# Kernel tuning notes

Hardware: AMD Instinct MI355X
Metric: run time of the kernel (lower is better)

The kernel has to match this reference:

```python
import jax, jax.numpy as jnp
import numpy as np
import math

STRIDES = [4, 8, 16, 32, 64]
SCALES  = [32, 64, 128, 256, 512]
RATIOS  = [2.0, 1.0, 0.5]
GRIDS   = [(200, 304), (100, 152), (50, 76), (25, 38), (13, 19)]  # 800x1216 canvas
LSZ     = [gh * gw * 3 for gh, gw in GRIDS]                        # anchors per level
PRE_NMS_K = [min(1000, n) for n in LSZ]                            # select_by_score (1000, lsz)
IMG_H, IMG_W = 800, 1216
BBOX_CLAMP = math.log(1000.0 / 16.0)
IOU_TH = 0.7
MAX_OUT = 1000
MIN_SIZE = 1e-2
LEVEL_OFFSET = 1e4  # batched-NMS level separation offset


def _make_priors():
    # post.get_priors with loc='corner': anchor centers at stride*i (no +0.5)
    out = []
    for st, (gh, gw), sc in zip(STRIDES, GRIDS, SCALES):
        anc = []
        for r in RATIOS:  # make_anchors_rounded: 1 scale x 3 ratios, rounded
            h = sc * np.sqrt(r)
            w = sc / np.sqrt(r)
            anc.append(np.round(np.array([-w / 2, -h / 2, w / 2, h / 2])))
        anc = np.stack(anc)  # [3,4]
        ys = (np.arange(gh) * st).astype(np.float32)
        xs = (np.arange(gw) * st).astype(np.float32)
        yy, xx = np.meshgrid(ys, xs, indexing='ij')
        shifts = np.stack([xx, yy, xx, yy], axis=-1).reshape(-1, 1, 4)  # [gh*gw,1,4]
        out.append((shifts + anc[None].astype(np.float32)).reshape(-1, 4))
    return np.concatenate(out).astype(np.float32)  # [A,4]


def setup_inputs() -> dict:
    key = jax.random.key(0)
    k1, k2 = jax.random.split(key)
    B, A = 16, sum(LSZ)
    reg = jax.random.normal(k1, (B, A, 4), dtype=jnp.float32) * 0.5  # box deltas
    obj = jax.random.normal(k2, (B, A, 1), dtype=jnp.float32)        # objectness logits
    priors = jnp.asarray(_make_priors())
    return {"reg": reg, "obj": obj, "priors": priors}


def _nms(boxes, init_keep):
    # sequential NMS over score-sorted boxes; boxes already level-offset. [N,4]
    N = boxes.shape[0]
    areas = jnp.clip(boxes[:, 2] - boxes[:, 0], 0) * jnp.clip(boxes[:, 3] - boxes[:, 1], 0)
    rng = jnp.arange(N)

    def body(i, keep):
        b = boxes[i]
        xx1 = jnp.maximum(b[0], boxes[:, 0])
        yy1 = jnp.maximum(b[1], boxes[:, 1])
        xx2 = jnp.minimum(b[2], boxes[:, 2])
        yy2 = jnp.minimum(b[3], boxes[:, 3])
        inter = jnp.clip(xx2 - xx1, 0) * jnp.clip(yy2 - yy1, 0)
        iou = inter / (areas[i] + areas - inter + 1e-9)
        sup = (iou > IOU_TH) & (rng > i) & keep[i]
        return keep & ~sup

    return jax.lax.fori_loop(0, N, body, init_keep)


def reference(reg, obj, priors):
    B = reg.shape[0]
    scores = jax.nn.sigmoid(obj[..., 0])  # [B,A]

    # per-level top-k selection (select_by_score with (1000, lsz))
    off = 0
    idxs, scs, levs = [], [], []
    for l, (n, k) in enumerate(zip(LSZ, PRE_NMS_K)):
        sv, si = jax.lax.top_k(scores[:, off:off + n], k)
        idxs.append(si + off)
        scs.append(sv)
        levs.append(np.full(k, l, np.int32))
        off += n
    idx = jnp.concatenate(idxs, axis=1)       # [B,N] global anchor indices
    sc = jnp.concatenate(scs, axis=1)         # [B,N]
    levels = jnp.asarray(np.concatenate(levs))  # [N]

    reg_s = jnp.take_along_axis(reg, idx[..., None], axis=1)  # [B,N,4]
    pri_s = priors[idx]                                        # [B,N,4]

    # decode_boxes, settings=(1, 1, log(1000/16))
    pw = pri_s[..., 2] - pri_s[..., 0]
    ph = pri_s[..., 3] - pri_s[..., 1]
    pcx = pri_s[..., 0] + 0.5 * pw
    pcy = pri_s[..., 1] + 0.5 * ph
    dx, dy = reg_s[..., 0], reg_s[..., 1]
    dw = jnp.minimum(reg_s[..., 2], BBOX_CLAMP)
    dh = jnp.minimum(reg_s[..., 3], BBOX_CLAMP)
    cx = dx * pw + pcx
    cy = dy * ph + pcy
    w = pw * jnp.exp(dw)
    h = ph * jnp.exp(dh)
    boxes = jnp.stack([cx - 0.5 * w, cy - 0.5 * h, cx + 0.5 * w, cy + 0.5 * h], axis=-1)

    # clamp_to_canvas
    boxes = jnp.stack([
        jnp.clip(boxes[..., 0], 0, IMG_W), jnp.clip(boxes[..., 1], 0, IMG_H),
        jnp.clip(boxes[..., 2], 0, IMG_W), jnp.clip(boxes[..., 3], 0, IMG_H)], axis=-1)

    # remove_small
    small_ok = ((boxes[..., 2] - boxes[..., 0]) > MIN_SIZE) & ((boxes[..., 3] - boxes[..., 1]) > MIN_SIZE)

    # global score-descending order for NMS
    order = jnp.argsort(-sc, axis=1)
    boxes = jnp.take_along_axis(boxes, order[..., None], axis=1)
    sc = jnp.take_along_axis(sc, order, axis=1)
    small_ok = jnp.take_along_axis(small_ok, order, axis=1)
    lev = jnp.take_along_axis(jnp.broadcast_to(levels, sc.shape), order, axis=1)

    # per-level batched NMS via coordinate offset; NMS decisions are non-differentiable
    boxes_off = jax.lax.stop_gradient(boxes) + lev[..., None].astype(boxes.dtype) * LEVEL_OFFSET
    keep = jax.vmap(_nms)(boxes_off, small_ok)  # [B,N] bool

    # take first MAX_OUT kept (already score-sorted), pad with zeros
    rank = jnp.cumsum(keep, axis=1) - 1
    pos = jnp.where(keep & (rank < MAX_OUT), rank, MAX_OUT)  # dump slot MAX_OUT
    out_b = jax.vmap(lambda p, b: jnp.zeros((MAX_OUT + 1, 4), b.dtype).at[p].set(b))(pos, boxes)[:, :MAX_OUT]
    out_s = jax.vmap(lambda p, s: jnp.zeros((MAX_OUT + 1,), s.dtype).at[p].set(s))(pos, sc)[:, :MAX_OUT]
    return jnp.concatenate([out_b, out_s[..., None]], axis=-1)  # [B,1000,5]
```

## Files before the change

kernel.cpp:

```cpp
#include <hip/hip_runtime.h>

typedef unsigned int u32;
typedef unsigned short u16;
typedef unsigned long long u64;

#define NB 16
#define NA 242991
#define NSEL 4741

__device__ __constant__ int c_LN[5]   = {182400, 45600, 11400, 2850, 741};
__device__ __constant__ int c_LOFF[5] = {0, 182400, 228000, 239400, 242250};
__device__ __constant__ int c_LK[5]   = {1000, 1000, 1000, 1000, 741};
__device__ __constant__ int c_SOFF[5] = {0, 1000, 2000, 3000, 4000};
__device__ __constant__ int c_CST[5]  = {0, 64, 80, 84, 85};
__device__ __constant__ int c_CCN[5]  = {64, 16, 4, 1, 1};


__device__ __forceinline__ float xla_tanhf(float x) {
#pragma clang fp contract(off)
  float t = fminf(fmaxf(x, -9.0f), 9.0f);
  float x2 = t * t;
  float p = -2.76076847742355e-16f;
  p = p * x2 + 2.00018790482477e-13f;
  p = p * x2 + -8.60467152213735e-11f;
  p = p * x2 + 5.12229709037114e-08f;
  p = p * x2 + 1.48572235717979e-05f;
  p = p * x2 + 6.37261928875436e-04f;
  p = p * x2 + 4.89352455891786e-03f;
  p = t * p;
  float q = 1.19825839466702e-06f;
  q = q * x2 + 1.18534705686654e-04f;
  q = q * x2 + 2.26843463243900e-03f;
  q = q * x2 + 4.89352518554385e-03f;
  float r = p / q;
  return (fabsf(x) < 0.0004f) ? x : r;
}

__device__ __forceinline__ float ref_sigmoid(float x) {
#pragma clang fp contract(off)
  float t = 0.5f * x;
  float th = xla_tanhf(t);
  return 0.5f + 0.5f * th;
}

__device__ __forceinline__ float xla_expf(float x) {
#pragma clang fp contract(off)
  float fx = x * 1.44269504088896341f + 0.5f;
  fx = floorf(fx);
  float tmp = fx * 0.693359375f;
  float z = fx * -2.12194440e-4f;
  float r = x - tmp;
  r = r - z;
  float r2 = r * r;
  float y = 1.9875691500e-4f;
  y = y * r + 1.3981999507e-3f;
  y = y * r + 8.3334519073e-3f;
  y = y * r + 4.1665795894e-2f;
  y = y * r + 1.6666665459e-1f;
  y = y * r + 5.0000001201e-1f;
  y = y * r2 + r;
  y = y + 1.0f;
  int k = (int)fx;
  float two_k = __uint_as_float((u32)((k + 127) << 23));
  return y * two_k;
}

__device__ __forceinline__ void chunk_map(int c, int& l, int& base, int& n) {
  if (c < 64)      { l = 0; base = c * 2850;                 n = 2850; }
  else if (c < 80) { l = 1; base = 182400 + (c - 64) * 2850; n = 2850; }
  else if (c < 84) { l = 2; base = 228000 + (c - 80) * 2850; n = 2850; }
  else if (c == 84){ l = 3; base = 239400;                   n = 2850; }
  else             { l = 4; base = 242250;                   n = 741;  }
}


__global__ void __launch_bounds__(256) k_hist(const float* __restrict__ obj,
                                              u16* __restrict__ ghist) {
  const int c = blockIdx.x, b = blockIdx.y;
  int l, base, n;
  chunk_map(c, l, base, n);
  __shared__ u32 h[4096];
  for (int i = threadIdx.x; i < 4096; i += 256) h[i] = 0;
  __syncthreads();
  const float* src = obj + (size_t)b * NA + base;
  for (int i = threadIdx.x; i < n; i += 256) {
    float s = ref_sigmoid(src[i]);
    atomicAdd(&h[__float_as_uint(s) >> 18], 1u);
  }
  __syncthreads();
  u32* gh = (u32*)(ghist + ((size_t)b * 86 + c) * 4096);
  for (int i = threadIdx.x; i < 2048; i += 256)
    gh[i] = (h[2 * i] & 0xFFFFu) | (h[2 * i + 1] << 16);
}


__global__ void __launch_bounds__(1024) k_thresh(const u16* __restrict__ ghist,
                                                 int2* __restrict__ binfo,
                                                 u32* __restrict__ ctrs) {
  const int l = blockIdx.x, b = blockIdx.y, t = threadIdx.x;
  const int K = c_LK[l];
  const int bl = b * 5 + l;
  if (t == 0) { ctrs[bl] = 0; ctrs[80 + bl] = 0; }
  __shared__ u32 scan[1024];
  __shared__ int sh_b;
  __shared__ u32 sh_G;
  u32 h0 = 0, h1 = 0, h2 = 0, h3 = 0;
  const int cs = c_CST[l], cn = c_CCN[l];
  const u16* base = ghist + (size_t)b * 86 * 4096 + 4 * t;
  for (int cc = 0; cc < cn; ++cc) {
    uint2 v = *(const uint2*)(base + (size_t)(cs + cc) * 4096);
    h0 += v.x & 0xFFFFu; h1 += v.x >> 16;
    h2 += v.y & 0xFFFFu; h3 += v.y >> 16;
  }
  u32 loc = h0 + h1 + h2 + h3;
  scan[t] = loc;
  __syncthreads();
  for (int d = 1; d < 1024; d <<= 1) {
    u32 v = (t + d < 1024) ? scan[t + d] : 0u;
    __syncthreads();
    scan[t] += v;
    __syncthreads();
  }
  u32 S = scan[t];
  u32 above = S - loc;
  if (S >= (u32)K && above < (u32)K) {
    u32 cacc = above;
    u32 cn2 = cacc + h3;
    if (cn2 >= (u32)K) { sh_b = 4 * t + 3; sh_G = cacc; }
    else {
      cacc = cn2; cn2 = cacc + h2;
      if (cn2 >= (u32)K) { sh_b = 4 * t + 2; sh_G = cacc; }
      else {
        cacc = cn2; cn2 = cacc + h1;
        if (cn2 >= (u32)K) { sh_b = 4 * t + 1; sh_G = cacc; }
        else { cacc = cn2; sh_b = 4 * t; sh_G = cacc; }
      }
    }
  }
  __syncthreads();
  if (t == 0) binfo[bl] = make_int2(sh_b, (int)sh_G);
}


__global__ void __launch_bounds__(256) k_emit(const float* __restrict__ obj,
                                              const int2* __restrict__ binfo,
                                              u64* __restrict__ skey,
                                              u64* __restrict__ candg,
                                              u32* __restrict__ ctrs) {
  const int c = blockIdx.x, b = blockIdx.y;
  int l, base, n;
  chunk_map(c, l, base, n);
  const int bl = b * 5 + l;
  const int bstar = binfo[bl].x;
  const float* src = obj + (size_t)b * NA + base;

  __shared__ u64 bufD[2880];
  __shared__ u64 bufC[2880];
  __shared__ u32 cntDC, gbD, gbC;
  if (threadIdx.x == 0) cntDC = 0;
  __syncthreads();

  const int lane = (int)threadIdx.x & 63;
  const u64 lmask_lt = (lane == 0) ? 0ull : ((~0ull) >> (64 - lane));
  const int iters = (n + 255) >> 8;
  for (int it = 0; it < iters; ++it) {
    int i = it * 256 + (int)threadIdx.x;
    bool valid = i < n;
    float s = ref_sigmoid(valid ? src[i] : 0.0f);
    u32 bits = __float_as_uint(s);
    int bin = (int)(bits >> 18);
    bool isD = valid && (bin > bstar);
    bool isC = valid && (bin == bstar);
    u64 mD = __ballot(isD);
    u64 mC = __ballot(isC);
    u32 bDC = 0;
    if (lane == 0) {
      u32 add = (u32)__popcll(mD) | ((u32)__popcll(mC) << 16);
      if (add) bDC = atomicAdd(&cntDC, add);
    }
    bDC = (u32)__shfl((int)bDC, 0, 64);
    u64 key = ((u64)(bits ^ 0xFFFFFFFFu) << 32) | (u32)(base + i);
    if (isD) bufD[(bDC & 0xFFFFu) + (u32)__popcll(mD & lmask_lt)] = key;
    if (isC) bufC[(bDC >> 16) + (u32)__popcll(mC & lmask_lt)] = key;
  }
  __syncthreads();
  const u32 nD = cntDC & 0xFFFFu, nC = cntDC >> 16;
  if (threadIdx.x == 0) {
    gbD = atomicAdd(&ctrs[bl], nD);
    gbC = atomicAdd(&ctrs[80 + bl], nC);
  }
  __syncthreads();
  const u32 gD = gbD, gC = gbC;
  u64* dstD = skey + (size_t)b * NSEL + c_SOFF[l] + gD;
  for (u32 i = threadIdx.x; i < nD; i += 256) dstD[i] = bufD[i];
  u64* dstC = candg + (size_t)bl * 2048;
  for (u32 i = threadIdx.x; i < nC; i += 256) {
    u32 p = gC + i;
    if (p < 2048) dstC[p] = bufC[i];
  }
}


__device__ __forceinline__ u64 shflx64(u64 v, int d) {
  u32 lo = (u32)v, hi = (u32)(v >> 32);
  lo = (u32)__shfl_xor((int)lo, d, 64);
  hi = (u32)__shfl_xor((int)hi, d, 64);
  return ((u64)hi << 32) | (u64)lo;
}

__global__ void __launch_bounds__(1024) k_selsort(
    const u64* __restrict__ candg, const int2* __restrict__ binfo,
    const u32* __restrict__ ctrs, u64* __restrict__ skey,
    const float* __restrict__ reg, const float* __restrict__ priors,
    float* __restrict__ boxes, float* __restrict__ scoref,
    float* __restrict__ nmsbox, u64* __restrict__ sow) {
  const int l = blockIdx.x, b = blockIdx.y, t = threadIdx.x;
  const int bl = b * 5 + l;
  const int K = c_LK[l];
  const int G = binfo[bl].y;
  u32 cc = ctrs[80 + bl];
  if (cc > 2048) cc = 2048;
  __shared__ u64 sm[4096];
  __shared__ u64 sh_sow[16];
  if (t < 16) sh_sow[t] = 0ull;
  const u64* seg = skey + (size_t)b * NSEL + c_SOFF[l];
  const u64* cnd = candg + (size_t)bl * 2048;

  const int total = G + (int)cc;
  const int NS = (total <= 2048) ? 2048 : 4096;
  const int Q = NS >> 2;
  const bool act = (t < Q);
  const int i0 = 4 * t;

  u64 v0 = ~0ull, v1 = ~0ull, v2 = ~0ull, v3 = ~0ull;
  if (act) {
    auto ld = [&](int i) -> u64 {
      if (i < G) return seg[i];
      int ci = i - G;
      return (ci < (int)cc) ? cnd[ci] : ~0ull;
    };
    v0 = ld(i0); v1 = ld(i0 + 1); v2 = ld(i0 + 2); v3 = ld(i0 + 3);
  }

  auto cs = [](u64& a, u64& b2, bool up) {
    if ((a > b2) == up) { u64 x = a; a = b2; b2 = x; }
  };

  if (act) {
    cs(v0, v1, true);
    cs(v2, v3, false);
    bool up = ((i0 & 4) == 0);
    cs(v0, v2, up); cs(v1, v3, up);
    cs(v0, v1, up); cs(v2, v3, up);
  }
  for (int k = 8; k <= NS; k <<= 1) {
    const bool up = ((i0 & k) == 0);
    for (int j = k >> 1; j >= 256; j >>= 1) {
      if (act) { sm[t] = v0; sm[Q + t] = v1; sm[2 * Q + t] = v2; sm[3 * Q + t] = v3; }
      __syncthreads();
      if (act) {
        const int u = t ^ (j >> 2);
        u64 o0 = sm[u], o1 = sm[Q + u], o2 = sm[2 * Q + u], o3 = sm[3 * Q + u];
        const bool keepmin = (((i0 & j) == 0) == up);
        v0 = keepmin ? (v0 < o0 ? v0 : o0) : (v0 > o0 ? v0 : o0);
        v1 = keepmin ? (v1 < o1 ? v1 : o1) : (v1 > o1 ? v1 : o1);
        v2 = keepmin ? (v2 < o2 ? v2 : o2) : (v2 > o2 ? v2 : o2);
        v3 = keepmin ? (v3 < o3 ? v3 : o3) : (v3 > o3 ? v3 : o3);
      }
      __syncthreads();
    }
    if (act) {
      int jstart = (k >> 1) < 128 ? (k >> 1) : 128;
      for (int j = jstart; j >= 4; j >>= 1) {
        const int d = j >> 2;
        const bool keepmin = (((t & d) == 0) == up);
        u64 o0 = shflx64(v0, d);
        u64 o1 = shflx64(v1, d);
        u64 o2 = shflx64(v2, d);
        u64 o3 = shflx64(v3, d);
        v0 = keepmin ? (v0 < o0 ? v0 : o0) : (v0 > o0 ? v0 : o0);
        v1 = keepmin ? (v1 < o1 ? v1 : o1) : (v1 > o1 ? v1 : o1);
        v2 = keepmin ? (v2 < o2 ? v2 : o2) : (v2 > o2 ? v2 : o2);
        v3 = keepmin ? (v3 < o3 ? v3 : o3) : (v3 > o3 ? v3 : o3);
      }
      cs(v0, v2, up); cs(v1, v3, up);
      cs(v0, v1, up); cs(v2, v3, up);
    }
  }

  u64* dst = skey + (size_t)b * NSEL + c_SOFF[l];

  {
#pragma clang fp contract(off)
    const float lf = (float)l * 10000.0f;
    u64 kv[4] = {v0, v1, v2, v3};
#pragma unroll
    for (int e = 0; e < 4; ++e) {
      int r = i0 + e;
      if (r < K) {
        u64 kk = kv[e];
        dst[r] = kk;
        u32 idx = (u32)kk;
        if (idx >= (u32)NA) idx = NA - 1;
        u32 bits = (u32)(kk >> 32) ^ 0xFFFFFFFFu;
        float s = __uint_as_float(bits);
        float4 r4 = ((const float4*)reg)[(size_t)b * NA + idx];
        float4 q4 = ((const float4*)priors)[idx];
        float pw = q4.z - q4.x;
        float ph = q4.w - q4.y;
        float pcx = q4.x + 0.5f * pw;
        float pcy = q4.y + 0.5f * ph;
        float dw = fminf(r4.z, 4.135166556742356f);
        float dh = fminf(r4.w, 4.135166556742356f);
        float cx = r4.x * pw + pcx;
        float cy = r4.y * ph + pcy;
        float w = pw * xla_expf(dw);
        float h = ph * xla_expf(dh);
        float x1 = cx - 0.5f * w;
        float y1 = cy - 0.5f * h;
        float x2 = cx + 0.5f * w;
        float y2 = cy + 0.5f * h;
        x1 = fminf(fmaxf(x1, 0.0f), 1216.0f);
        y1 = fminf(fmaxf(y1, 0.0f), 800.0f);
        x2 = fminf(fmaxf(x2, 0.0f), 1216.0f);
        y2 = fminf(fmaxf(y2, 0.0f), 800.0f);
        bool ok = ((x2 - x1) > 0.01f) && ((y2 - y1) > 0.01f);
        int sidx = c_SOFF[l] + r;
        ((float4*)boxes)[(size_t)b * NSEL + sidx] = make_float4(x1, y1, x2, y2);
        scoref[(size_t)b * NSEL + sidx] = s;
        ((float4*)nmsbox)[(size_t)(b * 5 + l) * 1000 + r] =
            make_float4(x1 + lf, y1 + lf, x2 + lf, y2 + lf);
        if (ok) atomicOr(&sh_sow[r >> 6], 1ull << (r & 63));
      }
    }
  }
  __syncthreads();
  if (t < 16) sow[(size_t)b * 80 + l * 16 + t] = sh_sow[t];
}


__device__ __forceinline__ void tile_map(int k, int& l, int& ti, int& tj) {
  int W;
  if (k < 544) { l = k / 136; k -= l * 136; W = 16; }
  else         { l = 4; k -= 544; W = 12; }
  int a = 0;
  while (k >= W - a) { k -= W - a; a++; }
  ti = a; tj = a + k;
}

__global__ void __launch_bounds__(256) k_nms_build(const float* __restrict__ nmsbox,
                                                   u64* __restrict__ mk) {
#pragma clang fp contract(off)
  const int b = blockIdx.y;
  const int wv = (int)threadIdx.x >> 6;
  const int tid = blockIdx.x * 4 + wv;
  __shared__ float4 cbox[4][64];
  __shared__ float car[4][64];
  if (tid >= 622) return;
  const int lane = (int)threadIdx.x & 63;
  int l, ti, tj;
  tile_map(tid, l, ti, tj);
  const int N = c_LK[l];
  const int bl = b * 5 + l;
  const float4* src = (const float4*)(nmsbox + (size_t)bl * 4000);
  const int i = ti * 64 + lane;
  const int j = tj * 64 + lane;
  const int il = (i < N) ? i : (N - 1);
  const int jl = (j < N) ? j : (N - 1);
  float4 rb = src[il];
  float4 cb0 = src[jl];
  float ra = fmaxf(rb.z - rb.x, 0.0f) * fmaxf(rb.w - rb.y, 0.0f);
  float ca0 = fmaxf(cb0.z - cb0.x, 0.0f) * fmaxf(cb0.w - cb0.y, 0.0f);
  cbox[wv][lane] = cb0;
  car[wv][lane] = ca0;
  u32 mlo = 0u, mhi = 0u;
  const double M = 0.7000000178813934326171875;
#pragma unroll
  for (int c = 0; c < 64; ++c) {
    float4 cb = cbox[wv][c];
    float xx1 = fmaxf(rb.x, cb.x);
    float yy1 = fmaxf(rb.y, cb.y);
    float xx2 = fminf(rb.z, cb.z);
    float yy2 = fminf(rb.w, cb.w);
    float inter = fmaxf(xx2 - xx1, 0.0f) * fmaxf(yy2 - yy1, 0.0f);
    if (__any(inter > 0.0f)) {
      float aj = car[wv][c];
      float den = ((ra + aj) - inter) + 1e-9f;
      bool sup = ((double)inter >= M * (double)den);
      if (c < 32) mlo |= sup ? (1u << c) : 0u;
      else        mhi |= sup ? (1u << (c - 32)) : 0u;
    }
  }
  u64 m = ((u64)mhi << 32) | (u64)mlo;
  if (ti == tj) m &= (lane == 63) ? 0ull : (~0ull << (lane + 1));
  int nc = N - tj * 64;
  if (nc < 64) m &= (1ull << nc) - 1ull;
  if (i < N) mk[(size_t)bl * 16000 + (size_t)tj * 1000 + i] = m;
}


__global__ void __launch_bounds__(1024) k_nms_scan(const u64* __restrict__ mk,
                                                   const u64* __restrict__ sow,
                                                   u64* __restrict__ keepw) {
  const int bl = blockIdx.x;
  const int b = bl / 5, l = bl % 5;
  const int N = c_LK[l];
  const int W = (N + 63) >> 6;
  const int lane = (int)threadIdx.x & 63;
  const int w = (int)threadIdx.x >> 6;
  const bool act = (w < W);
  __shared__ u64 sh_kept[16];

  const u64* rowp = mk + (size_t)bl * 16000 + (size_t)w * 1000;
  u64 acc = act ? ~sow[(size_t)b * 80 + l * 16 + w] : 0ull;

  u64 diag = 0ull;
  if (act) {
    int rd = w * 64 + lane;
    if (rd < N) diag = rowp[rd];
  }
  u64 nxt = (act && w > 0) ? rowp[lane] : 0ull;

  for (int g = 0; g < 16; ++g) {
    if (g >= W) break;
    u64 cur = nxt;
    if (act && w > g + 1) {
      int r = (g + 1) * 64 + lane;
      nxt = (r < N) ? rowp[r] : 0ull;
    } else {
      nxt = 0ull;
    }
    if (w == g) {
      u64 sup = acc;
      u64 pend = __ballot(diag != 0) & ~sup;
      while (pend) {
        int i = __builtin_ctzll(pend);
        u64 rr = __shfl(diag, i, 64);
        sup |= rr;
        pend &= ~sup;
        pend &= ~(1ull << i);
      }
      acc = sup;
      if (lane == 0) sh_kept[g] = ~sup;
    }
    __syncthreads();
    if (act && w > g) {
      u64 K = sh_kept[g];
      u64 c = ((K >> lane) & 1ull) ? cur : 0ull;
#pragma unroll
      for (int d = 1; d < 64; d <<= 1) c |= __shfl_xor(c, d, 64);
      acc |= c;
    }
    __syncthreads();
  }
  if (act && lane == 0) keepw[(size_t)b * 80 + l * 16 + w] = ~acc;
}


__global__ void __launch_bounds__(1024) k_out(const float* __restrict__ boxes,
                                              const float* __restrict__ scoref,
                                              const u64* __restrict__ skey,
                                              const u64* __restrict__ keepw,
                                              float* __restrict__ out) {
  const int l = blockIdx.x, b = blockIdx.y, t = threadIdx.x;
  __shared__ u64 sk[NSEL];
  __shared__ u64 kw[80];
  __shared__ u32 pp[5][17];
  __shared__ u32 sh_T;
  for (int i = t; i < NSEL; i += 1024) sk[i] = skey[(size_t)b * NSEL + i];
  if (t < 80) {
    int l2 = t >> 4, w = t & 15;
    int W = (c_LK[l2] + 63) >> 6;
    kw[t] = (w < W) ? keepw[(size_t)b * 80 + t] : 0ull;
  }
  __syncthreads();
  if (t < 5) {
    u32 acc = 0;
    pp[t][0] = 0;
    for (int w = 0; w < 16; ++w) {
      acc += (u32)__popcll(kw[t * 16 + w]);
      pp[t][w + 1] = acc;
    }
  }
  __syncthreads();
  if (t == 0) sh_T = pp[0][16] + pp[1][16] + pp[2][16] + pp[3][16] + pp[4][16];
  __syncthreads();
  const u32 T = sh_T;
  const int K = c_LK[l];

  for (int r = t; r < K; r += 1024) {
    int s = c_SOFF[l] + r;
    u64 word = kw[l * 16 + (r >> 6)];
    if ((word >> (r & 63)) & 1ull) {
      u32 rank = pp[l][r >> 6] +
                 (u32)__popcll(word & ((r & 63) ? ((1ull << (r & 63)) - 1ull) : 0ull));
      u64 key = sk[s];
#pragma unroll
      for (int l2 = 0; l2 < 5; ++l2) {
        if (l2 == l) continue;
        int lo = 0, hi = c_LK[l2];
        const int base2 = c_SOFF[l2];
        while (lo < hi) {
          int mid = (lo + hi) >> 1;
          if (sk[base2 + mid] < key) lo = mid + 1; else hi = mid;
        }
        u64 w2 = kw[l2 * 16 + (lo >> 6)];
        rank += pp[l2][lo >> 6] +
                (u32)__popcll(w2 & ((lo & 63) ? ((1ull << (lo & 63)) - 1ull) : 0ull));
      }
      if (rank < 1000u) {
        float4 bo = ((const float4*)boxes)[(size_t)b * NSEL + s];
        float* o = out + ((size_t)b * 1000 + rank) * 5;
        o[0] = bo.x; o[1] = bo.y; o[2] = bo.z; o[3] = bo.w;
        o[4] = scoref[(size_t)b * NSEL + s];
      }
    }
  }
  if (l == 0) {
    u32 start = (T < 1000u) ? T : 1000u;
    for (u32 i = start + t; i < 1000u; i += 1024u) {
      float* o = out + ((size_t)b * 1000 + i) * 5;
      o[0] = 0.0f; o[1] = 0.0f; o[2] = 0.0f; o[3] = 0.0f; o[4] = 0.0f;
    }
  }
}


extern "C" void kernel_launch(void* const* d_in, const int* in_sizes, int n_in,
                              void* d_out, int out_size, void* d_ws, size_t ws_size,
                              hipStream_t stream) {
  const float* reg = (const float*)d_in[0];
  const float* obj = (const float*)d_in[1];
  const float* priors = (const float*)d_in[2];
  float* out = (float*)d_out;

  char* ws = (char*)d_ws;
  size_t off = 0;
  auto alloc = [&](size_t bytes) {
    size_t r = off;
    off += (bytes + 255) & ~(size_t)255;
    return r;
  };
  u16* ghist = (u16*)(ws + alloc((size_t)NB * 86 * 4096 * 2));
  u32* ctrs = (u32*)(ws + alloc(160 * 4));
  int2* binfo = (int2*)(ws + alloc(80 * 8));
  u64* candg = (u64*)(ws + alloc((size_t)80 * 2048 * 8));
  u64* skey = (u64*)(ws + alloc((size_t)NB * NSEL * 8));
  float* boxes = (float*)(ws + alloc((size_t)NB * NSEL * 16));
  float* scoref = (float*)(ws + alloc((size_t)NB * NSEL * 4));
  float* nmsbox = (float*)(ws + alloc((size_t)NB * 5 * 1000 * 16));
  u64* sow = (u64*)(ws + alloc((size_t)NB * 80 * 8));
  u64* keepw = (u64*)(ws + alloc((size_t)NB * 80 * 8));
  u64* mk = (u64*)(ws + alloc((size_t)80 * 1000 * 16 * 8));

  k_hist<<<dim3(86, NB), 256, 0, stream>>>(obj, ghist);
  k_thresh<<<dim3(5, NB), 1024, 0, stream>>>(ghist, binfo, ctrs);
  k_emit<<<dim3(86, NB), 256, 0, stream>>>(obj, binfo, skey, candg, ctrs);
  k_selsort<<<dim3(5, NB), 1024, 0, stream>>>(candg, binfo, ctrs, skey, reg,
                                              priors, boxes, scoref, nmsbox, sow);
  k_nms_build<<<dim3(156, NB), 256, 0, stream>>>(nmsbox, mk);
  k_nms_scan<<<dim3(80), 1024, 0, stream>>>(mk, sow, keepw);
  k_out<<<dim3(5, NB), 1024, 0, stream>>>(boxes, scoref, skey, keepw, out);
}
```

Measured before the change: 112.4 us.

## Fuse NMS scan and output kernels with per-batch completion counter

Merges the NMS scan and output-gather kernels into one launch. Each level block signals completion through an atomic per-batch counter, and the level-0 block spin-waits on that counter before ranking and writing all 4741 slots. This removes one launch and its dependency gap, but serializes the output gather into one block per batch and relies on all blocks being co-resident to avoid deadlock. It also shrinks the emit shared buffers to raise occupancy, adds a 1024-element sort size, and uses DPP moves instead of shuffles for the small bitonic strides.

```diff
diff --git a/kernel.cpp b/kernel.cpp
--- a/kernel.cpp
+++ b/kernel.cpp
@@ -96,11 +96,12 @@
 
 __global__ void __launch_bounds__(1024) k_thresh(const u16* __restrict__ ghist,
                                                  int2* __restrict__ binfo,
-                                                 u32* __restrict__ ctrs) {
+                                                 u32* __restrict__ ctrs,
+                                                 u32* __restrict__ done) {
   const int l = blockIdx.x, b = blockIdx.y, t = threadIdx.x;
   const int K = c_LK[l];
   const int bl = b * 5 + l;
-  if (t == 0) { ctrs[bl] = 0; ctrs[80 + bl] = 0; }
+  if (t == 0) { ctrs[bl] = 0; ctrs[80 + bl] = 0; if (l == 0) done[b] = 0; }
   __shared__ u32 scan[1024];
   __shared__ int sh_b;
   __shared__ u32 sh_G;
@@ -154,8 +155,8 @@
   const int bstar = binfo[bl].x;
   const float* src = obj + (size_t)b * NA + base;
 
-  __shared__ u64 bufD[2880];
-  __shared__ u64 bufC[2880];
+  __shared__ u64 bufD[1024];
+  __shared__ u64 bufC[2048];
   __shared__ u32 cntDC, gbD, gbC;
   if (threadIdx.x == 0) cntDC = 0;
   __syncthreads();
@@ -180,8 +181,14 @@
     }
     bDC = (u32)__shfl((int)bDC, 0, 64);
     u64 key = ((u64)(bits ^ 0xFFFFFFFFu) << 32) | (u32)(base + i);
-    if (isD) bufD[(bDC & 0xFFFFu) + (u32)__popcll(mD & lmask_lt)] = key;
-    if (isC) bufC[(bDC >> 16) + (u32)__popcll(mC & lmask_lt)] = key;
+    if (isD) {
+      u32 p = (bDC & 0xFFFFu) + (u32)__popcll(mD & lmask_lt);
+      if (p < 1024) bufD[p] = key;
+    }
+    if (isC) {
+      u32 p = (bDC >> 16) + (u32)__popcll(mC & lmask_lt);
+      if (p < 2048) bufC[p] = key;
+    }
   }
   __syncthreads();
   const u32 nD = cntDC & 0xFFFFu, nC = cntDC >> 16;
@@ -196,7 +203,7 @@
   u64* dstC = candg + (size_t)bl * 2048;
   for (u32 i = threadIdx.x; i < nC; i += 256) {
     u32 p = gC + i;
-    if (p < 2048) dstC[p] = bufC[i];
+    if (p < 2048 && i < 2048) dstC[p] = bufC[i];
   }
 }
 
@@ -205,6 +212,13 @@
   u32 lo = (u32)v, hi = (u32)(v >> 32);
   lo = (u32)__shfl_xor((int)lo, d, 64);
   hi = (u32)__shfl_xor((int)hi, d, 64);
+  return ((u64)hi << 32) | (u64)lo;
+}
+
+template <int CTRL>
+__device__ __forceinline__ u64 dpp64(u64 v) {
+  u32 lo = (u32)__builtin_amdgcn_mov_dpp((int)(u32)v, CTRL, 0xF, 0xF, true);
+  u32 hi = (u32)__builtin_amdgcn_mov_dpp((int)(u32)(v >> 32), CTRL, 0xF, 0xF, true);
   return ((u64)hi << 32) | (u64)lo;
 }
 
@@ -227,7 +241,7 @@
   const u64* cnd = candg + (size_t)bl * 2048;
 
   const int total = G + (int)cc;
-  const int NS = (total <= 2048) ? 2048 : 4096;
+  const int NS = (total <= 1024) ? 1024 : (total <= 2048) ? 2048 : 4096;
   const int Q = NS >> 2;
   const bool act = (t < Q);
   const int i0 = 4 * t;
@@ -273,11 +287,18 @@
       int jstart = (k >> 1) < 128 ? (k >> 1) : 128;
       for (int j = jstart; j >= 4; j >>= 1) {
         const int d = j >> 2;
+        u64 o0, o1, o2, o3;
+        if (d == 1) {
+          o0 = dpp64<0xB1>(v0); o1 = dpp64<0xB1>(v1);
+          o2 = dpp64<0xB1>(v2); o3 = dpp64<0xB1>(v3);
+        } else if (d == 2) {
+          o0 = dpp64<0x4E>(v0); o1 = dpp64<0x4E>(v1);
+          o2 = dpp64<0x4E>(v2); o3 = dpp64<0x4E>(v3);
+        } else {
+          o0 = shflx64(v0, d); o1 = shflx64(v1, d);
+          o2 = shflx64(v2, d); o3 = shflx64(v3, d);
+        }
         const bool keepmin = (((t & d) == 0) == up);
-        u64 o0 = shflx64(v0, d);
-        u64 o1 = shflx64(v1, d);
-        u64 o2 = shflx64(v2, d);
-        u64 o3 = shflx64(v3, d);
         v0 = keepmin ? (v0 < o0 ? v0 : o0) : (v0 > o0 ? v0 : o0);
         v1 = keepmin ? (v1 < o1 ? v1 : o1) : (v1 > o1 ? v1 : o1);
         v2 = keepmin ? (v2 < o2 ? v2 : o2) : (v2 > o2 ? v2 : o2);
@@ -399,74 +420,80 @@
 }
 
 
-__global__ void __launch_bounds__(1024) k_nms_scan(const u64* __restrict__ mk,
-                                                   const u64* __restrict__ sow,
-                                                   u64* __restrict__ keepw) {
-  const int bl = blockIdx.x;
-  const int b = bl / 5, l = bl % 5;
-  const int N = c_LK[l];
-  const int W = (N + 63) >> 6;
-  const int lane = (int)threadIdx.x & 63;
-  const int w = (int)threadIdx.x >> 6;
-  const bool act = (w < W);
-  __shared__ u64 sh_kept[16];
-
-  const u64* rowp = mk + (size_t)bl * 16000 + (size_t)w * 1000;
-  u64 acc = act ? ~sow[(size_t)b * 80 + l * 16 + w] : 0ull;
-
-  u64 diag = 0ull;
-  if (act) {
-    int rd = w * 64 + lane;
-    if (rd < N) diag = rowp[rd];
-  }
-  u64 nxt = (act && w > 0) ? rowp[lane] : 0ull;
-
-  for (int g = 0; g < 16; ++g) {
-    if (g >= W) break;
-    u64 cur = nxt;
-    if (act && w > g + 1) {
-      int r = (g + 1) * 64 + lane;
-      nxt = (r < N) ? rowp[r] : 0ull;
-    } else {
-      nxt = 0ull;
-    }
-    if (w == g) {
-      u64 sup = acc;
-      u64 pend = __ballot(diag != 0) & ~sup;
-      while (pend) {
-        int i = __builtin_ctzll(pend);
-        u64 rr = __shfl(diag, i, 64);
-        sup |= rr;
-        pend &= ~sup;
-        pend &= ~(1ull << i);
-      }
-      acc = sup;
-      if (lane == 0) sh_kept[g] = ~sup;
-    }
-    __syncthreads();
-    if (act && w > g) {
-      u64 K = sh_kept[g];
-      u64 c = ((K >> lane) & 1ull) ? cur : 0ull;
-#pragma unroll
-      for (int d = 1; d < 64; d <<= 1) c |= __shfl_xor(c, d, 64);
-      acc |= c;
-    }
-    __syncthreads();
-  }
-  if (act && lane == 0) keepw[(size_t)b * 80 + l * 16 + w] = ~acc;
-}
-
-
-__global__ void __launch_bounds__(1024) k_out(const float* __restrict__ boxes,
-                                              const float* __restrict__ scoref,
-                                              const u64* __restrict__ skey,
-                                              const u64* __restrict__ keepw,
-                                              float* __restrict__ out) {
+__global__ void __launch_bounds__(1024, 4) k_scanout(
+    const u64* __restrict__ mk, const u64* __restrict__ sow,
+    u64* __restrict__ keepw, u32* __restrict__ done,
+    const float* __restrict__ boxes, const float* __restrict__ scoref,
+    const u64* __restrict__ skey, float* __restrict__ out) {
   const int l = blockIdx.x, b = blockIdx.y, t = threadIdx.x;
+  const int bl = b * 5 + l;
   __shared__ u64 sk[NSEL];
   __shared__ u64 kw[80];
   __shared__ u32 pp[5][17];
   __shared__ u32 sh_T;
+  __shared__ u64 sh_kept[16];
+
+  {
+    const int N = c_LK[l];
+    const int W = (N + 63) >> 6;
+    const int lane = t & 63;
+    const int w = t >> 6;
+    const bool act = (w < W);
+    const u64* rowp = mk + (size_t)bl * 16000 + (size_t)w * 1000;
+    u64 acc = act ? ~sow[(size_t)b * 80 + l * 16 + w] : 0ull;
+    u64 diag = 0ull;
+    if (act) {
+      int rd = w * 64 + lane;
+      if (rd < N) diag = rowp[rd];
+    }
+    u64 nxt = (act && w > 0) ? rowp[lane] : 0ull;
+    for (int g = 0; g < 16; ++g) {
+      if (g >= W) break;
+      u64 cur = nxt;
+      if (act && w > g + 1) {
+        int r = (g + 1) * 64 + lane;
+        nxt = (r < N) ? rowp[r] : 0ull;
+      } else {
+        nxt = 0ull;
+      }
+      if (w == g) {
+        u64 sup = acc;
+        u64 pend = __ballot(diag != 0) & ~sup;
+        while (pend) {
+          int i = __builtin_ctzll(pend);
+          u64 rr = __shfl(diag, i, 64);
+          sup |= rr;
+          pend &= ~sup;
+          pend &= ~(1ull << i);
+        }
+        acc = sup;
+        if (lane == 0) sh_kept[g] = ~sup;
+      }
+      __syncthreads();
+      if (act && w > g) {
+        u64 Kk = sh_kept[g];
+        u64 c = ((Kk >> lane) & 1ull) ? cur : 0ull;
+#pragma unroll
+        for (int d = 1; d < 64; d <<= 1) c |= __shfl_xor(c, d, 64);
+        acc |= c;
+      }
+      __syncthreads();
+    }
+    if (act && lane == 0) keepw[(size_t)b * 80 + l * 16 + w] = ~acc;
+  }
+  __syncthreads();
+  if (t == 0) {
+    __threadfence();
+    atomicAdd(&done[b], 1u);
+  }
+  if (l != 0) return;
+
+  if (t == 0) {
+    while (atomicAdd(&done[b], 0u) < 5u) { }
+  }
+  __syncthreads();
+  __threadfence();
+
   for (int i = t; i < NSEL; i += 1024) sk[i] = skey[(size_t)b * NSEL + i];
   if (t < 80) {
     int l2 = t >> 4, w = t & 15;
@@ -486,26 +513,26 @@
   if (t == 0) sh_T = pp[0][16] + pp[1][16] + pp[2][16] + pp[3][16] + pp[4][16];
   __syncthreads();
   const u32 T = sh_T;
-  const int K = c_LK[l];
-
-  for (int r = t; r < K; r += 1024) {
-    int s = c_SOFF[l] + r;
-    u64 word = kw[l * 16 + (r >> 6)];
+
+  for (int s = t; s < NSEL; s += 1024) {
+    int l2 = (s >= 4000) ? 4 : (s / 1000);
+    int r = s - c_SOFF[l2];
+    u64 word = kw[l2 * 16 + (r >> 6)];
     if ((word >> (r & 63)) & 1ull) {
-      u32 rank = pp[l][r >> 6] +
+      u32 rank = pp[l2][r >> 6] +
                  (u32)__popcll(word & ((r & 63) ? ((1ull << (r & 63)) - 1ull) : 0ull));
       u64 key = sk[s];
 #pragma unroll
-      for (int l2 = 0; l2 < 5; ++l2) {
-        if (l2 == l) continue;
-        int lo = 0, hi = c_LK[l2];
-        const int base2 = c_SOFF[l2];
+      for (int l3 = 0; l3 < 5; ++l3) {
+        if (l3 == l2) continue;
+        int lo = 0, hi = c_LK[l3];
+        const int base2 = c_SOFF[l3];
         while (lo < hi) {
           int mid = (lo + hi) >> 1;
           if (sk[base2 + mid] < key) lo = mid + 1; else hi = mid;
         }
-        u64 w2 = kw[l2 * 16 + (lo >> 6)];
-        rank += pp[l2][lo >> 6] +
+        u64 w2 = kw[l3 * 16 + (lo >> 6)];
+        rank += pp[l3][lo >> 6] +
                 (u32)__popcll(w2 & ((lo & 63) ? ((1ull << (lo & 63)) - 1ull) : 0ull));
       }
       if (rank < 1000u) {
@@ -516,12 +543,10 @@
       }
     }
   }
-  if (l == 0) {
-    u32 start = (T < 1000u) ? T : 1000u;
-    for (u32 i = start + t; i < 1000u; i += 1024u) {
-      float* o = out + ((size_t)b * 1000 + i) * 5;
-      o[0] = 0.0f; o[1] = 0.0f; o[2] = 0.0f; o[3] = 0.0f; o[4] = 0.0f;
-    }
+  u32 start = (T < 1000u) ? T : 1000u;
+  for (u32 i = start + t; i < 1000u; i += 1024u) {
+    float* o = out + ((size_t)b * 1000 + i) * 5;
+    o[0] = 0.0f; o[1] = 0.0f; o[2] = 0.0f; o[3] = 0.0f; o[4] = 0.0f;
   }
 }
 
@@ -543,6 +568,7 @@
   };
   u16* ghist = (u16*)(ws + alloc((size_t)NB * 86 * 4096 * 2));
   u32* ctrs = (u32*)(ws + alloc(160 * 4));
+  u32* done = (u32*)(ws + alloc(NB * 4));
   int2* binfo = (int2*)(ws + alloc(80 * 8));
   u64* candg = (u64*)(ws + alloc((size_t)80 * 2048 * 8));
   u64* skey = (u64*)(ws + alloc((size_t)NB * NSEL * 8));
@@ -554,11 +580,11 @@
   u64* mk = (u64*)(ws + alloc((size_t)80 * 1000 * 16 * 8));
 
   k_hist<<<dim3(86, NB), 256, 0, stream>>>(obj, ghist);
-  k_thresh<<<dim3(5, NB), 1024, 0, stream>>>(ghist, binfo, ctrs);
+  k_thresh<<<dim3(5, NB), 1024, 0, stream>>>(ghist, binfo, ctrs, done);
   k_emit<<<dim3(86, NB), 256, 0, stream>>>(obj, binfo, skey, candg, ctrs);
   k_selsort<<<dim3(5, NB), 1024, 0, stream>>>(candg, binfo, ctrs, skey, reg,
                                               priors, boxes, scoref, nmsbox, sow);
   k_nms_build<<<dim3(156, NB), 256, 0, stream>>>(nmsbox, mk);
-  k_nms_scan<<<dim3(80), 1024, 0, stream>>>(mk, sow, keepw);
-  k_out<<<dim3(5, NB), 1024, 0, stream>>>(boxes, scoref, skey, keepw, out);
-}
+  k_scanout<<<dim3(5, NB), 1024, 0, stream>>>(mk, sow, keepw, done, boxes,
+                                              scoref, skey, out);
+}
```

Measured after the change: 126.2 us. 1.12x slower.

## Shrink emit LDS buffers, add 1024-wide sort tier, use DPP for short shuffles

Applied to the files above, without the earlier changes.

The emit kernel's shared buffers shrink from 2880 to 1024 and 2048 entries, with bounds checks on writes, to cut LDS use and allow more blocks per CU. The selection sort gets a 1024-element tier so small candidate sets run fewer bitonic stages. In-wave exchanges at distance 1 and 2 use DPP quad permutes instead of ds_bpermute-based shuffles. The smaller D buffer risks silently dropping keys if more than 1024 definite entries land in one chunk.

```diff
diff --git a/kernel.cpp b/kernel.cpp
--- a/kernel.cpp
+++ b/kernel.cpp
@@ -154,8 +154,8 @@
   const int bstar = binfo[bl].x;
   const float* src = obj + (size_t)b * NA + base;
 
-  __shared__ u64 bufD[2880];
-  __shared__ u64 bufC[2880];
+  __shared__ u64 bufD[1024];
+  __shared__ u64 bufC[2048];
   __shared__ u32 cntDC, gbD, gbC;
   if (threadIdx.x == 0) cntDC = 0;
   __syncthreads();
@@ -180,8 +180,14 @@
     }
     bDC = (u32)__shfl((int)bDC, 0, 64);
     u64 key = ((u64)(bits ^ 0xFFFFFFFFu) << 32) | (u32)(base + i);
-    if (isD) bufD[(bDC & 0xFFFFu) + (u32)__popcll(mD & lmask_lt)] = key;
-    if (isC) bufC[(bDC >> 16) + (u32)__popcll(mC & lmask_lt)] = key;
+    if (isD) {
+      u32 p = (bDC & 0xFFFFu) + (u32)__popcll(mD & lmask_lt);
+      if (p < 1024) bufD[p] = key;
+    }
+    if (isC) {
+      u32 p = (bDC >> 16) + (u32)__popcll(mC & lmask_lt);
+      if (p < 2048) bufC[p] = key;
+    }
   }
   __syncthreads();
   const u32 nD = cntDC & 0xFFFFu, nC = cntDC >> 16;
@@ -196,7 +202,7 @@
   u64* dstC = candg + (size_t)bl * 2048;
   for (u32 i = threadIdx.x; i < nC; i += 256) {
     u32 p = gC + i;
-    if (p < 2048) dstC[p] = bufC[i];
+    if (p < 2048 && i < 2048) dstC[p] = bufC[i];
   }
 }
 
@@ -205,6 +211,13 @@
   u32 lo = (u32)v, hi = (u32)(v >> 32);
   lo = (u32)__shfl_xor((int)lo, d, 64);
   hi = (u32)__shfl_xor((int)hi, d, 64);
+  return ((u64)hi << 32) | (u64)lo;
+}
+
+template <int CTRL>
+__device__ __forceinline__ u64 dpp64(u64 v) {
+  u32 lo = (u32)__builtin_amdgcn_mov_dpp((int)(u32)v, CTRL, 0xF, 0xF, true);
+  u32 hi = (u32)__builtin_amdgcn_mov_dpp((int)(u32)(v >> 32), CTRL, 0xF, 0xF, true);
   return ((u64)hi << 32) | (u64)lo;
 }
 
@@ -227,7 +240,7 @@
   const u64* cnd = candg + (size_t)bl * 2048;
 
   const int total = G + (int)cc;
-  const int NS = (total <= 2048) ? 2048 : 4096;
+  const int NS = (total <= 1024) ? 1024 : (total <= 2048) ? 2048 : 4096;
   const int Q = NS >> 2;
   const bool act = (t < Q);
   const int i0 = 4 * t;
@@ -273,11 +286,18 @@
       int jstart = (k >> 1) < 128 ? (k >> 1) : 128;
       for (int j = jstart; j >= 4; j >>= 1) {
         const int d = j >> 2;
+        u64 o0, o1, o2, o3;
+        if (d == 1) {
+          o0 = dpp64<0xB1>(v0); o1 = dpp64<0xB1>(v1);
+          o2 = dpp64<0xB1>(v2); o3 = dpp64<0xB1>(v3);
+        } else if (d == 2) {
+          o0 = dpp64<0x4E>(v0); o1 = dpp64<0x4E>(v1);
+          o2 = dpp64<0x4E>(v2); o3 = dpp64<0x4E>(v3);
+        } else {
+          o0 = shflx64(v0, d); o1 = shflx64(v1, d);
+          o2 = shflx64(v2, d); o3 = shflx64(v3, d);
+        }
         const bool keepmin = (((t & d) == 0) == up);
-        u64 o0 = shflx64(v0, d);
-        u64 o1 = shflx64(v1, d);
-        u64 o2 = shflx64(v2, d);
-        u64 o3 = shflx64(v3, d);
         v0 = keepmin ? (v0 < o0 ? v0 : o0) : (v0 > o0 ? v0 : o0);
         v1 = keepmin ? (v1 < o1 ? v1 : o1) : (v1 > o1 ? v1 : o1);
         v2 = keepmin ? (v2 < o2 ? v2 : o2) : (v2 > o2 ? v2 : o2);
```

Result: faster. 109.4 us (-2.6%).
